# Performance work log

Measured on AMD Instinct MI355X. Metric: run time of the kernel, lower is better.

Reference implementation:

```python
import jax, jax.numpy as jnp
import numpy as np

D_MODEL = 512
N_HEADS = 8
D_K = D_MODEL // N_HEADS  # 64
MAX_LEN = 5000


def _positional_encoding(d_model, max_len):
    pe = np.zeros((max_len, d_model), dtype=np.float32)
    position = np.arange(max_len, dtype=np.float32)[:, None]
    div_term = np.exp(np.arange(0, d_model, 2, dtype=np.float32) * (-np.log(10000.0) / d_model))
    pe[:, 0::2] = np.sin(position * div_term)
    pe[:, 1::2] = np.cos(position * div_term)
    return jnp.asarray(pe)


def _layer_norm(x, gamma, beta, eps):
    mu = jnp.mean(x, axis=-1, keepdims=True)
    var = jnp.mean(jnp.square(x - mu), axis=-1, keepdims=True)
    return (x - mu) * jax.lax.rsqrt(var + eps) * gamma + beta


def setup_inputs() -> dict:
    key = jax.random.key(0)
    ks = jax.random.split(key, 5)
    s = 1.0 / np.sqrt(D_MODEL)
    return {
        "x": jax.random.normal(ks[0], (4, 2048, D_MODEL), dtype=jnp.float32),
        "ln1_g": jnp.ones((D_MODEL,), jnp.float32),
        "ln1_b": jnp.zeros((D_MODEL,), jnp.float32),
        "wq": jax.random.normal(ks[1], (D_MODEL, D_MODEL), jnp.float32) * s,
        "wk": jax.random.normal(ks[2], (D_MODEL, D_MODEL), jnp.float32) * s,
        "wv": jax.random.normal(ks[3], (D_MODEL, D_MODEL), jnp.float32) * s,
        "wfc": jax.random.normal(ks[4], (D_MODEL, D_MODEL), jnp.float32) * s,
        "ln2_g": jnp.ones((D_MODEL,), jnp.float32),
        "ln2_b": jnp.zeros((D_MODEL,), jnp.float32),
    }


def reference(x, ln1_g, ln1_b, wq, wk, wv, wfc, ln2_g, ln2_b):
    B, T, D = x.shape
    residual0 = x
    # outer pre-norm (nn.LayerNorm default eps=1e-5)
    h = _layer_norm(x, ln1_g, ln1_b, 1e-5)
    # sinusoidal positional encoding
    h = h + _positional_encoding(D_MODEL, MAX_LEN)[:T]
    residual1 = h
    # projections -> [B, H, T, d]
    q = (h @ wq).reshape(B, T, N_HEADS, D_K).transpose(0, 2, 1, 3)
    k = (h @ wk).reshape(B, T, N_HEADS, D_K).transpose(0, 2, 1, 3)
    v = (h @ wv).reshape(B, T, N_HEADS, D_K).transpose(0, 2, 1, 3)
    scale = 1.0 / np.sqrt(D_K).astype(np.float32)
    attn = jnp.einsum("bhqd,bhkd->bhqk", q * scale, k)
    causal = jnp.tril(jnp.ones((T, T), dtype=bool))  # subsequent mask
    attn = jnp.where(causal, attn, jnp.float32(-1e9))
    attn = jax.nn.softmax(attn, axis=-1)
    o = jnp.einsum("bhqk,bhkd->bhqd", attn, v)
    o = o.transpose(0, 2, 1, 3).reshape(B, T, D)
    o = o @ wfc
    # inner post-attention residual + LayerNorm (eps=1e-6)
    h2 = _layer_norm(o + residual1, ln2_g, ln2_b, 1e-6)
    return h2 + residual0
```

## Files before the change

### kernel.cpp

```cpp
#include <hip/hip_runtime.h>
#include <hip/hip_bf16.h>

#define B_ 4
#define T_ 2048
#define D_ 512

typedef __attribute__((ext_vector_type(8))) short short8;
typedef __attribute__((ext_vector_type(4))) short short4v;
typedef __attribute__((ext_vector_type(4))) float float4v;
typedef unsigned short bf16_t;

__device__ __forceinline__ bf16_t f2bf(float f) {
  unsigned int u = __builtin_bit_cast(unsigned int, f);
  unsigned int r = (u + 0x7fffu + ((u >> 16) & 1u)) >> 16;
  return (bf16_t)r;
}
__device__ __forceinline__ float bf2f(bf16_t b) {
  unsigned int u = ((unsigned int)b) << 16;
  return __builtin_bit_cast(float, u);
}

__device__ __forceinline__ float fast_exp2(float x) {
#if __has_builtin(__builtin_amdgcn_exp2f)
  return __builtin_amdgcn_exp2f(x);
#else
  float r;
  asm("v_exp_f32 %0, %1" : "=v"(r) : "v"(x));
  return r;
#endif
}

__device__ __forceinline__ unsigned cvt_pk_bf16(float lo, float hi) {
  unsigned r;
  asm("v_cvt_pk_bf16_f32 %0, %1, %2" : "=v"(r) : "v"(lo), "v"(hi));
  return r;
}

__device__ __forceinline__ float waveReduceSum(float v) {
#pragma unroll
  for (int m = 32; m >= 1; m >>= 1) v += __shfl_xor(v, m, 64);
  return v;
}

__device__ __forceinline__ void gld16(const bf16_t* g, bf16_t* l) {
  __builtin_amdgcn_global_load_lds(
      (const __attribute__((address_space(1))) void*)g,
      (__attribute__((address_space(3))) void*)l, 16, 0, 0);
}

__global__ __launch_bounds__(256) void pre_kernel(
    const float* __restrict__ x, const float* __restrict__ g,
    const float* __restrict__ bb,
    const float* __restrict__ wq, const float* __restrict__ wk,
    const float* __restrict__ wv, const float* __restrict__ wfc,
    bf16_t* __restrict__ h_bf16,
    bf16_t* __restrict__ wqkvT, bf16_t* __restrict__ wfcT) {
  if (blockIdx.x >= 2048) {
    int bid = blockIdx.x - 2048;
#pragma unroll 4
    for (int i = 0; i < 16; ++i) {
      int idx = bid * 4096 + i * 256 + threadIdx.x;
      if (idx < 786432) {
        int n = idx >> 9, k = idx & 511;
        const float* src = (n < 512) ? wq : ((n < 1024) ? wk : wv);
        float scl = (n < 512) ? 1.4426950408889634f
                              : ((n < 1024) ? 0.125f : 1.0f);
        int c = n & 511;
        wqkvT[idx] = f2bf(src[k * 512 + c] * scl);
      } else {
        int j = idx - 786432;
        int n = j >> 9, k = j & 511;
        wfcT[j] = f2bf(wfc[k * 512 + n]);
      }
    }
    return;
  }
  int wave = threadIdx.x >> 6, lane = threadIdx.x & 63;
  int row = blockIdx.x * 4 + wave;
  int pos = row & (T_ - 1);
  const float* xr = x + (size_t)row * D_;
  int c0 = lane * 8;
  float v[8];
  float4 a = *(const float4*)(xr + c0);
  float4 b4 = *(const float4*)(xr + c0 + 4);
  v[0]=a.x; v[1]=a.y; v[2]=a.z; v[3]=a.w;
  v[4]=b4.x; v[5]=b4.y; v[6]=b4.z; v[7]=b4.w;
  float s = 0.f;
#pragma unroll
  for (int j = 0; j < 8; ++j) s += v[j];
  s = waveReduceSum(s);
  float mu = s * (1.f / 512.f);
  float q = 0.f;
#pragma unroll
  for (int j = 0; j < 8; ++j) { float d = v[j] - mu; q += d * d; }
  q = waveReduceSum(q);
  float rstd = rsqrtf(q * (1.f / 512.f) + 1e-5f);
  bf16_t* hb = h_bf16 + (size_t)row * D_;
  float fpos = (float)pos;
#pragma unroll
  for (int jp = 0; jp < 4; ++jp) {
    int col = c0 + jp * 2;
    float dt = fast_exp2((float)col * (-13.287712379549449f / 512.0f));
    float ang = fpos * dt;
    float hn0 = (v[2 * jp] - mu) * rstd * g[col] + bb[col] + __sinf(ang);
    float hn1 = (v[2 * jp + 1] - mu) * rstd * g[col + 1] + bb[col + 1] + __cosf(ang);
    hb[col] = f2bf(hn0);
    hb[col + 1] = f2bf(hn1);
  }
}

template <typename EPI>
__device__ __forceinline__ void gemm_body(const bf16_t* __restrict__ A,
                                          const bf16_t* __restrict__ Bt,
                                          int m0, int n0, bf16_t* As, bf16_t* Bs,
                                          EPI epi) {
  const int tid = threadIdx.x;
  const int w = tid >> 6, lane = tid & 63;
  const int ln = lane & 15, quad = lane >> 4;
  const int wy = w >> 1, wx = w & 1;
  const int sw = ln & 7;

  float4v acc[4][4];
  float4v z = {0.f, 0.f, 0.f, 0.f};
#pragma unroll
  for (int i = 0; i < 4; ++i)
#pragma unroll
    for (int j = 0; j < 4; ++j) acc[i][j] = z;

  for (int k0 = 0; k0 < 512; k0 += 64) {
#pragma unroll
    for (int i = 0; i < 4; ++i) {
      int cbase = w * 256 + i * 64;
      int chunk = cbase + lane;
      int row = chunk >> 3;
      int lb = (chunk & 7) ^ (row & 7);
      gld16(A + (size_t)(m0 + row) * 512 + k0 + lb * 8, As + cbase * 8);
      gld16(Bt + (size_t)(n0 + row) * 512 + k0 + lb * 8, Bs + cbase * 8);
    }
    __syncthreads();
#pragma unroll
    for (int c = 0; c < 2; ++c) {
      short8 af[4], bf[4];
#pragma unroll
      for (int mt = 0; mt < 4; ++mt)
        af[mt] = *(const short8*)(As + (wy * 64 + mt * 16 + ln) * 64 + (((c * 4 + quad) ^ sw)) * 8);
#pragma unroll
      for (int nt = 0; nt < 4; ++nt)
        bf[nt] = *(const short8*)(Bs + (wx * 64 + nt * 16 + ln) * 64 + (((c * 4 + quad) ^ sw)) * 8);
#pragma unroll
      for (int mt = 0; mt < 4; ++mt)
#pragma unroll
        for (int nt = 0; nt < 4; ++nt)
          acc[mt][nt] = __builtin_amdgcn_mfma_f32_16x16x32_bf16(af[mt], bf[nt], acc[mt][nt], 0, 0, 0);
    }
    __syncthreads();
  }
#pragma unroll
  for (int mt = 0; mt < 4; ++mt)
#pragma unroll
    for (int r = 0; r < 4; ++r) {
      int row = m0 + wy * 64 + mt * 16 + quad * 4 + r;
#pragma unroll
      for (int nt = 0; nt < 4; ++nt) {
        int col = n0 + wx * 64 + nt * 16 + ln;
        epi(row, col, acc[mt][nt][r]);
      }
    }
}

__global__ __launch_bounds__(256) void gemm_qkvt_kernel(
    const bf16_t* __restrict__ h_bf, const bf16_t* __restrict__ wqkvT,
    bf16_t* __restrict__ qk, bf16_t* __restrict__ vT) {
  __shared__ __align__(16) bf16_t As[128 * 64];
  __shared__ __align__(16) bf16_t Bs[128 * 64];
  int bx = blockIdx.x;
  if (bx < 512) {
    int m0 = (bx >> 3) * 128, n0 = (bx & 7) * 128;
    gemm_body(h_bf, wqkvT, m0, n0, As, Bs,
              [&](int row, int col, float v) { qk[(size_t)row * 1024 + col] = f2bf(v); });
  } else {
    int local = bx - 512;
    int m0 = (local >> 6) * 128, n0 = (local & 63) * 128;
    gemm_body(wqkvT + 1024 * 512, h_bf, m0, n0, As, Bs,
              [&](int row, int col, float v) { vT[(size_t)row * 8192 + col] = f2bf(v); });
  }
}

__global__ __launch_bounds__(256) void gemm_out_kernel(
    const bf16_t* __restrict__ attn, const bf16_t* __restrict__ wfcT,
    const bf16_t* __restrict__ h_bf, bf16_t* __restrict__ o2r) {
  __shared__ __align__(16) bf16_t As[128 * 64];
  __shared__ __align__(16) bf16_t Bs[128 * 64];
  int bx = blockIdx.x;
  int m0 = (bx >> 2) * 128, n0 = (bx & 3) * 128;
  gemm_body(attn, wfcT, m0, n0, As, Bs, [&](int row, int col, float v) {
    size_t o = (size_t)row * 512 + col;
    o2r[o] = f2bf(v + bf2f(h_bf[o]));
  });
}

__global__ __launch_bounds__(256) void attn_kernel(const bf16_t* __restrict__ qk,
                                                   const bf16_t* __restrict__ vT,
                                                   bf16_t* __restrict__ p0,
                                                   bf16_t* __restrict__ p1,
                                                   float2* __restrict__ stats) {
  __shared__ __align__(16) bf16_t Ks[2][64 * 64];
  __shared__ __align__(16) bf16_t Vs[2][64 * 64];
  const int bx = blockIdx.x;
  const int qt = 31 - (bx >> 6);
  const int rest = bx & 63;
  const int half = rest & 1;
  const int bh = rest >> 1;
  const int b = bh >> 3, h = bh & 7;
  const int tid = threadIdx.x;
  const int w = tid >> 6, lane = tid & 63;
  const int ln = lane & 15, quad = lane >> 4;
  const int sw = ln & 7;

  const int nlo = (qt + 2) >> 1;
  const int kt0 = half ? nlo : 0;
  const int ktN = half ? (qt + 1) : nlo;

  short8 qf0, qf1;
  {
    size_t qrow = ((size_t)b * T_ + qt * 64 + w * 16 + ln) * 1024 + h * 64;
    qf0 = *(const short8*)(qk + qrow + quad * 8);
    qf1 = *(const short8*)(qk + qrow + 32 + quad * 8);
  }
  float4v z = {0.f, 0.f, 0.f, 0.f};
  float4v oacc[4];
#pragma unroll
  for (int i = 0; i < 4; ++i) oacc[i] = z;
  float m_s = -1e30f, l_s = 0.f;

  const bf16_t* kbase = qk + (size_t)b * T_ * 1024 + 512 + h * 64;
  const bf16_t* vbase = vT + (size_t)(h * 64) * 8192 + (size_t)b * T_;

  const int cb0 = w * 128, cb1 = w * 128 + 64;
  const int ch0 = cb0 + lane, ch1 = cb1 + lane;
  const int r0 = ch0 >> 3, r1 = ch1 >> 3;
  const int lb0 = (ch0 & 7) ^ (r0 & 7), lb1 = (ch1 & 7) ^ (r1 & 7);
  const bf16_t* kg0 = kbase + (size_t)(kt0 * 64 + r0) * 1024 + lb0 * 8;
  const bf16_t* kg1 = kbase + (size_t)(kt0 * 64 + r1) * 1024 + lb1 * 8;
  const bf16_t* vg0 = vbase + (size_t)r0 * 8192 + kt0 * 64 + lb0 * 8;
  const bf16_t* vg1 = vbase + (size_t)r1 * 8192 + kt0 * 64 + lb1 * 8;

  auto stage2 = [&](int buf) {
    gld16(kg0, Ks[buf] + cb0 * 8);
    gld16(kg1, Ks[buf] + cb1 * 8);
    gld16(vg0, Vs[buf] + cb0 * 8);
    gld16(vg1, Vs[buf] + cb1 * 8);
    kg0 += 64 * 1024; kg1 += 64 * 1024;
    vg0 += 64;        vg1 += 64;
  };

  auto compute = [&](const bf16_t* Kc, const bf16_t* Vc, bool mask) {
    float sv[4][4];
#pragma unroll
    for (int mt = 0; mt < 4; ++mt) {
      float4v st = z;
      int row = mt * 16 + ln;
      short8 a0 = *(const short8*)(Kc + row * 64 + ((0 + quad) ^ sw) * 8);
      short8 a1 = *(const short8*)(Kc + row * 64 + ((4 + quad) ^ sw) * 8);
      st = __builtin_amdgcn_mfma_f32_16x16x32_bf16(a0, qf0, st, 0, 0, 0);
      st = __builtin_amdgcn_mfma_f32_16x16x32_bf16(a1, qf1, st, 0, 0, 0);
#pragma unroll
      for (int r = 0; r < 4; ++r) {
        float v = st[r];
        if (mask) {
          int kloc = mt * 16 + quad * 4 + r;
          if (kloc > w * 16 + ln) v = -1e30f;
        }
        sv[mt][r] = v;
      }
    }
    float mxa[4];
#pragma unroll
    for (int mt = 0; mt < 4; ++mt)
      mxa[mt] = fmaxf(fmaxf(sv[mt][0], sv[mt][1]), fmaxf(sv[mt][2], sv[mt][3]));
    float mx = fmaxf(fmaxf(mxa[0], mxa[1]), fmaxf(mxa[2], mxa[3]));
    mx = fmaxf(mx, __shfl_xor(mx, 16, 64));
    mx = fmaxf(mx, __shfl_xor(mx, 32, 64));
    if (!__all(mx <= m_s + 8.0f)) {
      float mn = fmaxf(m_s, mx);
      float alpha = fast_exp2(m_s - mn);
      m_s = mn;
      l_s *= alpha;
#pragma unroll
      for (int dt = 0; dt < 4; ++dt)
#pragma unroll
        for (int r = 0; r < 4; ++r) oacc[dt][r] *= alpha;
    }
    float rsa[4];
#pragma unroll
    for (int mt = 0; mt < 4; ++mt) {
#pragma unroll
      for (int r = 0; r < 4; ++r) sv[mt][r] = fast_exp2(sv[mt][r] - m_s);
      rsa[mt] = (sv[mt][0] + sv[mt][1]) + (sv[mt][2] + sv[mt][3]);
    }
    float rs = (rsa[0] + rsa[1]) + (rsa[2] + rsa[3]);
    rs += __shfl_xor(rs, 16, 64);
    rs += __shfl_xor(rs, 32, 64);
    l_s += rs;
    short4v pf[4];
#pragma unroll
    for (int mt = 0; mt < 4; ++mt) {
      uint2 pp;
      pp.x = cvt_pk_bf16(sv[mt][0], sv[mt][1]);
      pp.y = cvt_pk_bf16(sv[mt][2], sv[mt][3]);
      pf[mt] = __builtin_bit_cast(short4v, pp);
    }
#pragma unroll
    for (int dt = 0; dt < 4; ++dt) {
      int row = dt * 16 + ln;
#pragma unroll
      for (int mt = 0; mt < 4; ++mt) {
        short4v av = *(const short4v*)(Vc + row * 64 + ((2 * mt + (quad >> 1)) ^ sw) * 8 + (quad & 1) * 4);
        oacc[dt] = __builtin_amdgcn_mfma_f32_16x16x16bf16_1k(av, pf[mt], oacc[dt], 0, 0, 0);
      }
    }
  };

  if (ktN > kt0) {
    const int nt = ktN - kt0;
    stage2(0);
    __syncthreads();
    for (int i = 0; i < nt - 1; ++i) {
      int cur = i & 1;
      stage2(cur ^ 1);
      compute(Ks[cur], Vs[cur], false);
      __syncthreads();
    }
    compute(Ks[(nt - 1) & 1], Vs[(nt - 1) & 1], (ktN - 1) == qt);
  }

  bf16_t* dst = half ? p1 : p0;
  size_t obase = ((size_t)b * T_ + qt * 64 + w * 16 + ln) * 512 + h * 64;
#pragma unroll
  for (int dt = 0; dt < 4; ++dt) {
    short4v o4;
#pragma unroll
    for (int r = 0; r < 4; ++r) o4[r] = (short)f2bf(oacc[dt][r]);
    *(short4v*)(dst + obase + dt * 16 + quad * 4) = o4;
  }
  if (quad == 0) {
    int grow = b * T_ + qt * 64 + w * 16 + ln;
    float2 st; st.x = m_s; st.y = l_s;
    stats[half * 65536 + grow * 8 + h] = st;
  }
}

__global__ __launch_bounds__(256) void combine_kernel(
    bf16_t* __restrict__ p0, const bf16_t* __restrict__ p1,
    const float2* __restrict__ stats) {
  int wave = threadIdx.x >> 6, lane = threadIdx.x & 63;
  int row = blockIdx.x * 4 + wave;
  int h = lane >> 3;
  float2 s0 = stats[row * 8 + h];
  float2 s1 = stats[65536 + row * 8 + h];
  float m = fmaxf(s0.x, s1.x);
  float w0 = fast_exp2(s0.x - m), w1 = fast_exp2(s1.x - m);
  float inv = 1.0f / (s0.y * w0 + s1.y * w1);
  float a0 = w0 * inv, a1 = w1 * inv;
  size_t ro = (size_t)row * 512 + lane * 8;
  short8 l8 = *(const short8*)(p0 + ro);
  short8 h8 = *(const short8*)(p1 + ro);
  short8 o8;
#pragma unroll
  for (int j = 0; j < 8; ++j)
    o8[j] = (short)f2bf(bf2f((bf16_t)l8[j]) * a0 + bf2f((bf16_t)h8[j]) * a1);
  *(short8*)(p0 + ro) = o8;
}

__global__ __launch_bounds__(256) void ln2_kernel(
    const bf16_t* __restrict__ o2r, const float* __restrict__ x,
    const float* __restrict__ g, const float* __restrict__ bb,
    float* __restrict__ out) {
  int wave = threadIdx.x >> 6, lane = threadIdx.x & 63;
  int row = blockIdx.x * 4 + wave;
  size_t ro = (size_t)row * D_;
  int c0 = lane * 8;
  short8 ov = *(const short8*)(o2r + ro + c0);
  float t[8];
#pragma unroll
  for (int j = 0; j < 8; ++j) t[j] = bf2f((bf16_t)ov[j]);
  float s = 0.f;
#pragma unroll
  for (int j = 0; j < 8; ++j) s += t[j];
  s = waveReduceSum(s);
  float mu = s * (1.f / 512.f);
  float q = 0.f;
#pragma unroll
  for (int j = 0; j < 8; ++j) { float d = t[j] - mu; q += d * d; }
  q = waveReduceSum(q);
  float rstd = rsqrtf(q * (1.f / 512.f) + 1e-6f);
  float4 x0 = *(const float4*)(x + ro + c0);
  float4 x1 = *(const float4*)(x + ro + c0 + 4);
  float xr[8] = {x0.x, x0.y, x0.z, x0.w, x1.x, x1.y, x1.z, x1.w};
  float o[8];
#pragma unroll
  for (int j = 0; j < 8; ++j) {
    int col = c0 + j;
    o[j] = (t[j] - mu) * rstd * g[col] + bb[col] + xr[j];
  }
  float4 w0 = {o[0], o[1], o[2], o[3]};
  float4 w1 = {o[4], o[5], o[6], o[7]};
  *(float4*)(out + ro + c0) = w0;
  *(float4*)(out + ro + c0 + 4) = w1;
}

extern "C" void kernel_launch(void* const* d_in, const int* in_sizes, int n_in,
                              void* d_out, int out_size, void* d_ws, size_t ws_size,
                              hipStream_t stream) {
  const float* x   = (const float*)d_in[0];
  const float* g1  = (const float*)d_in[1];
  const float* b1  = (const float*)d_in[2];
  const float* wq  = (const float*)d_in[3];
  const float* wk  = (const float*)d_in[4];
  const float* wv  = (const float*)d_in[5];
  const float* wfc = (const float*)d_in[6];
  const float* g2  = (const float*)d_in[7];
  const float* b2  = (const float*)d_in[8];
  float* out = (float*)d_out;

  char* ws = (char*)d_ws;
  const size_t O_HBF  = 0;
  const size_t O_WQKV = 8388608;
  const size_t O_WFC  = 9961472;
  const size_t O_QK   = 10485760;
  const size_t O_VT   = 27262976;
  const size_t O_ATTN = 35651584;
  const size_t O_O2R  = 44040192;
  const size_t WS_NEED = 52428800;
  if (ws_size < WS_NEED) return;

  bf16_t* h_bf  = (bf16_t*)(ws + O_HBF);
  bf16_t* wqkvT = (bf16_t*)(ws + O_WQKV);
  bf16_t* wfcT  = (bf16_t*)(ws + O_WFC);
  bf16_t* qk    = (bf16_t*)(ws + O_QK);
  bf16_t* vT    = (bf16_t*)(ws + O_VT);
  bf16_t* attn  = (bf16_t*)(ws + O_ATTN);
  bf16_t* o2r   = (bf16_t*)(ws + O_O2R);
  float2* stats = (float2*)(ws + O_WQKV);

  pre_kernel<<<dim3(2304), dim3(256), 0, stream>>>(x, g1, b1, wq, wk, wv, wfc,
                                                   h_bf, wqkvT, wfcT);
  gemm_qkvt_kernel<<<dim3(768), dim3(256), 0, stream>>>(h_bf, wqkvT, qk, vT);
  attn_kernel<<<dim3(2048), dim3(256), 0, stream>>>(qk, vT, attn, o2r, stats);
  combine_kernel<<<dim3(2048), dim3(256), 0, stream>>>(attn, o2r, stats);
  gemm_out_kernel<<<dim3(256), dim3(256), 0, stream>>>(attn, wfcT, h_bf, o2r);
  ln2_kernel<<<dim3(2048), dim3(256), 0, stream>>>(o2r, x, g2, b2, out);
}
```

Measured before the change: 183.4 us.

## Process two query tiles per attention block to reuse staged K/V tiles

Each attention block now handles 128 query rows (two 64-row sub-tiles with separate softmax state) instead of 64, so every K/V tile staged into shared memory feeds both sub-tiles. The grid is halved and block indexing is reordered so that heads vary fastest, and launch bounds request 4 blocks per SM. This cuts global-to-LDS traffic and sync count per unit of work, at the cost of more registers per thread and some wasted work on the diagonal tile, where one sub-tile is inactive.

```diff
diff --git a/kernel.cpp b/kernel.cpp
--- a/kernel.cpp
+++ b/kernel.cpp
@@ -199,39 +199,43 @@
   });
 }
 
-__global__ __launch_bounds__(256) void attn_kernel(const bf16_t* __restrict__ qk,
-                                                   const bf16_t* __restrict__ vT,
-                                                   bf16_t* __restrict__ p0,
-                                                   bf16_t* __restrict__ p1,
-                                                   float2* __restrict__ stats) {
+__global__ __launch_bounds__(256, 4) void attn_kernel(const bf16_t* __restrict__ qk,
+                                                      const bf16_t* __restrict__ vT,
+                                                      bf16_t* __restrict__ p0,
+                                                      bf16_t* __restrict__ p1,
+                                                      float2* __restrict__ stats) {
   __shared__ __align__(16) bf16_t Ks[2][64 * 64];
   __shared__ __align__(16) bf16_t Vs[2][64 * 64];
   const int bx = blockIdx.x;
-  const int qt = 31 - (bx >> 6);
-  const int rest = bx & 63;
-  const int half = rest & 1;
-  const int bh = rest >> 1;
-  const int b = bh >> 3, h = bh & 7;
+  const int h = bx & 7;
+  const int slot = bx >> 3;
+  const int t = 15 - (slot >> 3);
+  const int b = (slot >> 1) & 3;
+  const int half = slot & 1;
   const int tid = threadIdx.x;
   const int w = tid >> 6, lane = tid & 63;
   const int ln = lane & 15, quad = lane >> 4;
   const int sw = ln & 7;
 
-  const int nlo = (qt + 2) >> 1;
+  const int Nt = 2 * t + 2;
+  const int nlo = t + 1;
   const int kt0 = half ? nlo : 0;
-  const int ktN = half ? (qt + 1) : nlo;
-
-  short8 qf0, qf1;
-  {
-    size_t qrow = ((size_t)b * T_ + qt * 64 + w * 16 + ln) * 1024 + h * 64;
-    qf0 = *(const short8*)(qk + qrow + quad * 8);
-    qf1 = *(const short8*)(qk + qrow + 32 + quad * 8);
+  const int ktN = half ? Nt : nlo;
+
+  short8 qf[2][2];
+#pragma unroll
+  for (int s = 0; s < 2; ++s) {
+    size_t qrow = ((size_t)b * T_ + t * 128 + s * 64 + w * 16 + ln) * 1024 + h * 64;
+    qf[s][0] = *(const short8*)(qk + qrow + quad * 8);
+    qf[s][1] = *(const short8*)(qk + qrow + 32 + quad * 8);
   }
   float4v z = {0.f, 0.f, 0.f, 0.f};
-  float4v oacc[4];
-#pragma unroll
-  for (int i = 0; i < 4; ++i) oacc[i] = z;
-  float m_s = -1e30f, l_s = 0.f;
+  float4v oacc[2][4];
+#pragma unroll
+  for (int s = 0; s < 2; ++s)
+#pragma unroll
+    for (int i = 0; i < 4; ++i) oacc[s][i] = z;
+  float m_s[2] = {-1e30f, -1e30f}, l_s[2] = {0.f, 0.f};
 
   const bf16_t* kbase = qk + (size_t)b * T_ * 1024 + 512 + h * 64;
   const bf16_t* vbase = vT + (size_t)(h * 64) * 8192 + (size_t)b * T_;
@@ -254,26 +258,7 @@
     vg0 += 64;        vg1 += 64;
   };
 
-  auto compute = [&](const bf16_t* Kc, const bf16_t* Vc, bool mask) {
-    float sv[4][4];
-#pragma unroll
-    for (int mt = 0; mt < 4; ++mt) {
-      float4v st = z;
-      int row = mt * 16 + ln;
-      short8 a0 = *(const short8*)(Kc + row * 64 + ((0 + quad) ^ sw) * 8);
-      short8 a1 = *(const short8*)(Kc + row * 64 + ((4 + quad) ^ sw) * 8);
-      st = __builtin_amdgcn_mfma_f32_16x16x32_bf16(a0, qf0, st, 0, 0, 0);
-      st = __builtin_amdgcn_mfma_f32_16x16x32_bf16(a1, qf1, st, 0, 0, 0);
-#pragma unroll
-      for (int r = 0; r < 4; ++r) {
-        float v = st[r];
-        if (mask) {
-          int kloc = mt * 16 + quad * 4 + r;
-          if (kloc > w * 16 + ln) v = -1e30f;
-        }
-        sv[mt][r] = v;
-      }
-    }
+  auto softmax = [&](float sv[4][4], float& ms, float& ls, float4v* oa, short4v* pf) {
     float mxa[4];
 #pragma unroll
     for (int mt = 0; mt < 4; ++mt)
@@ -281,28 +266,27 @@
     float mx = fmaxf(fmaxf(mxa[0], mxa[1]), fmaxf(mxa[2], mxa[3]));
     mx = fmaxf(mx, __shfl_xor(mx, 16, 64));
     mx = fmaxf(mx, __shfl_xor(mx, 32, 64));
-    if (!__all(mx <= m_s + 8.0f)) {
-      float mn = fmaxf(m_s, mx);
-      float alpha = fast_exp2(m_s - mn);
-      m_s = mn;
-      l_s *= alpha;
+    if (!__all(mx <= ms + 8.0f)) {
+      float mn = fmaxf(ms, mx);
+      float alpha = fast_exp2(ms - mn);
+      ms = mn;
+      ls *= alpha;
 #pragma unroll
       for (int dt = 0; dt < 4; ++dt)
 #pragma unroll
-        for (int r = 0; r < 4; ++r) oacc[dt][r] *= alpha;
+        for (int r = 0; r < 4; ++r) oa[dt][r] *= alpha;
     }
     float rsa[4];
 #pragma unroll
     for (int mt = 0; mt < 4; ++mt) {
 #pragma unroll
-      for (int r = 0; r < 4; ++r) sv[mt][r] = fast_exp2(sv[mt][r] - m_s);
+      for (int r = 0; r < 4; ++r) sv[mt][r] = fast_exp2(sv[mt][r] - ms);
       rsa[mt] = (sv[mt][0] + sv[mt][1]) + (sv[mt][2] + sv[mt][3]);
     }
     float rs = (rsa[0] + rsa[1]) + (rsa[2] + rsa[3]);
     rs += __shfl_xor(rs, 16, 64);
     rs += __shfl_xor(rs, 32, 64);
-    l_s += rs;
-    short4v pf[4];
+    ls += rs;
 #pragma unroll
     for (int mt = 0; mt < 4; ++mt) {
       uint2 pp;
@@ -310,43 +294,86 @@
       pp.y = cvt_pk_bf16(sv[mt][2], sv[mt][3]);
       pf[mt] = __builtin_bit_cast(short4v, pp);
     }
+  };
+
+  auto compute = [&](const bf16_t* Kc, const bf16_t* Vc,
+                     bool act0, bool mask0, bool mask1) {
+    float sv0[4][4], sv1[4][4];
+#pragma unroll
+    for (int mt = 0; mt < 4; ++mt) {
+      int row = mt * 16 + ln;
+      short8 a0 = *(const short8*)(Kc + row * 64 + ((0 + quad) ^ sw) * 8);
+      short8 a1 = *(const short8*)(Kc + row * 64 + ((4 + quad) ^ sw) * 8);
+      float4v st1 = z;
+      st1 = __builtin_amdgcn_mfma_f32_16x16x32_bf16(a0, qf[1][0], st1, 0, 0, 0);
+      st1 = __builtin_amdgcn_mfma_f32_16x16x32_bf16(a1, qf[1][1], st1, 0, 0, 0);
+      if (act0) {
+        float4v st0 = z;
+        st0 = __builtin_amdgcn_mfma_f32_16x16x32_bf16(a0, qf[0][0], st0, 0, 0, 0);
+        st0 = __builtin_amdgcn_mfma_f32_16x16x32_bf16(a1, qf[0][1], st0, 0, 0, 0);
+#pragma unroll
+        for (int r = 0; r < 4; ++r) {
+          float v = st0[r];
+          if (mask0) {
+            int kloc = mt * 16 + quad * 4 + r;
+            if (kloc > w * 16 + ln) v = -1e30f;
+          }
+          sv0[mt][r] = v;
+        }
+      }
+#pragma unroll
+      for (int r = 0; r < 4; ++r) {
+        float v = st1[r];
+        if (mask1) {
+          int kloc = mt * 16 + quad * 4 + r;
+          if (kloc > w * 16 + ln) v = -1e30f;
+        }
+        sv1[mt][r] = v;
+      }
+    }
+    short4v pf0[4], pf1[4];
+    if (act0) softmax(sv0, m_s[0], l_s[0], oacc[0], pf0);
+    softmax(sv1, m_s[1], l_s[1], oacc[1], pf1);
 #pragma unroll
     for (int dt = 0; dt < 4; ++dt) {
       int row = dt * 16 + ln;
 #pragma unroll
       for (int mt = 0; mt < 4; ++mt) {
         short4v av = *(const short4v*)(Vc + row * 64 + ((2 * mt + (quad >> 1)) ^ sw) * 8 + (quad & 1) * 4);
-        oacc[dt] = __builtin_amdgcn_mfma_f32_16x16x16bf16_1k(av, pf[mt], oacc[dt], 0, 0, 0);
+        if (act0)
+          oacc[0][dt] = __builtin_amdgcn_mfma_f32_16x16x16bf16_1k(av, pf0[mt], oacc[0][dt], 0, 0, 0);
+        oacc[1][dt] = __builtin_amdgcn_mfma_f32_16x16x16bf16_1k(av, pf1[mt], oacc[1][dt], 0, 0, 0);
       }
     }
   };
 
-  if (ktN > kt0) {
-    const int nt = ktN - kt0;
-    stage2(0);
-    __syncthreads();
-    for (int i = 0; i < nt - 1; ++i) {
-      int cur = i & 1;
-      stage2(cur ^ 1);
-      compute(Ks[cur], Vs[cur], false);
-      __syncthreads();
-    }
-    compute(Ks[(nt - 1) & 1], Vs[(nt - 1) & 1], (ktN - 1) == qt);
+  const int nt = ktN - kt0;
+  stage2(0);
+  __syncthreads();
+  for (int i = 0; i < nt; ++i) {
+    int cur = i & 1;
+    if (i + 1 < nt) stage2(cur ^ 1);
+    int jg = kt0 + i;
+    compute(Ks[cur], Vs[cur], jg <= 2 * t, jg == 2 * t, jg == 2 * t + 1);
+    if (i + 1 < nt) __syncthreads();
   }
 
   bf16_t* dst = half ? p1 : p0;
-  size_t obase = ((size_t)b * T_ + qt * 64 + w * 16 + ln) * 512 + h * 64;
-#pragma unroll
-  for (int dt = 0; dt < 4; ++dt) {
-    short4v o4;
-#pragma unroll
-    for (int r = 0; r < 4; ++r) o4[r] = (short)f2bf(oacc[dt][r]);
-    *(short4v*)(dst + obase + dt * 16 + quad * 4) = o4;
-  }
-  if (quad == 0) {
-    int grow = b * T_ + qt * 64 + w * 16 + ln;
-    float2 st; st.x = m_s; st.y = l_s;
-    stats[half * 65536 + grow * 8 + h] = st;
+#pragma unroll
+  for (int s = 0; s < 2; ++s) {
+    int qrow = b * T_ + t * 128 + s * 64 + w * 16 + ln;
+    size_t obase = (size_t)qrow * 512 + h * 64;
+#pragma unroll
+    for (int dt = 0; dt < 4; ++dt) {
+      short4v o4;
+#pragma unroll
+      for (int r = 0; r < 4; ++r) o4[r] = (short)f2bf(oacc[s][dt][r]);
+      *(short4v*)(dst + obase + dt * 16 + quad * 4) = o4;
+    }
+    if (quad == 0) {
+      float2 st; st.x = m_s[s]; st.y = l_s[s];
+      stats[half * 65536 + qrow * 8 + h] = st;
+    }
   }
 }
 
@@ -446,7 +473,7 @@
   pre_kernel<<<dim3(2304), dim3(256), 0, stream>>>(x, g1, b1, wq, wk, wv, wfc,
                                                    h_bf, wqkvT, wfcT);
   gemm_qkvt_kernel<<<dim3(768), dim3(256), 0, stream>>>(h_bf, wqkvT, qk, vT);
-  attn_kernel<<<dim3(2048), dim3(256), 0, stream>>>(qk, vT, attn, o2r, stats);
+  attn_kernel<<<dim3(1024), dim3(256), 0, stream>>>(qk, vT, attn, o2r, stats);
   combine_kernel<<<dim3(2048), dim3(256), 0, stream>>>(attn, o2r, stats);
   gemm_out_kernel<<<dim3(256), dim3(256), 0, stream>>>(attn, wfcT, h_bf, o2r);
   ln2_kernel<<<dim3(2048), dim3(256), 0, stream>>>(o2r, x, g2, b2, out);
```

Result: slower. 205.0 us (+11.8%).
